# Kernel optimization log

Hardware: AMD Instinct MI355X
Metric: run time of the kernel (lower is better)

## Reference

```python
import jax, jax.numpy as jnp
import numpy as np

B, L = 128, 1024
V, E, H = 32, 256, 1024


def setup_inputs() -> dict:
    key = jax.random.key(0)
    ks = jax.random.split(key, 6)
    return {
        "x": jax.random.randint(ks[0], (B, L), 0, V),
        "hidden": jnp.zeros((B, H), dtype=jnp.float32),
        "embedding": jax.random.normal(ks[1], (V, E), dtype=jnp.float32),
        "W_e": jax.random.normal(ks[2], (E, H), dtype=jnp.float32) * 0.01,
        "W_h": jax.random.normal(ks[3], (H, H), dtype=jnp.float32) * 0.01,
        "b_h": jnp.zeros((H,), dtype=jnp.float32),
        "W_o": jax.random.normal(ks[4], (H, V), dtype=jnp.float32) * 0.01,
        "b_o": jnp.zeros((V,), dtype=jnp.float32),
    }


def reference(x, hidden, embedding, W_e, W_h, b_h, W_o, b_o):
    # x: [B, L] int -> embed: [B, L, E]
    x_embed = embedding[x]
    # Precompute the input projection for all timesteps at once: [L, B, H]
    xin = jnp.einsum("ble,eh->lbh", x_embed, W_e) + b_h

    def step(h, x_t):
        # h: [B, H], x_t: [B, H] (already projected + bias)
        h_new = jnp.tanh(x_t + h @ W_h)
        return h_new, h_new

    final_hidden, outputs = jax.lax.scan(step, hidden, xin)
    # outputs: [L, B, H] -> [B, L, H]
    outputs = outputs.transpose(1, 0, 2)
    logits = outputs @ W_o + b_o  # [B, L, V]
    return logits, final_hidden
```

## Files before the change

### kernel.cpp

```cpp
#include <hip/hip_runtime.h>

typedef unsigned short u16;
typedef unsigned int   u32;
typedef __attribute__((ext_vector_type(4))) float floatx4;
typedef __attribute__((ext_vector_type(4))) u32  u32x4;
typedef __attribute__((ext_vector_type(8))) short short8;

#define B_SZ  128
#define L_SEQ 1024
#define V_SZ  32
#define E_SZ  256
#define H_SZ  1024

#define N_GROUPS     8
#define WG_PER_GROUP 8
#define N_BLOCKS     (N_GROUPS * WG_PER_GROUP)
#define LOGIT_BASE   (B_SZ * L_SEQ * V_SZ)

#define BAR_BYTES  8192
#define FLAG_OFF   (BAR_BYTES - 8)
#define P_OFF      BAR_BYTES
#define P_BYTES    (V_SZ * H_SZ * 4)
#define HBUF_OFF   (P_OFF + P_BYTES)
#define NBUF       4
#define HBUF_G     (NBUF * 16 * H_SZ)
#define HBUF_BYTES (N_GROUPS * HBUF_G * 2)

#define SENT 0xFFFFFFFFu

#define MFMA16x16x32(a, b, c) __builtin_amdgcn_mfma_f32_16x16x32_bf16(a, b, c, 0, 0, 0)

__device__ inline float b2f(u16 u) {
    union { unsigned i; float f; } x; x.i = ((unsigned)u) << 16; return x.f;
}
__device__ inline u16 f2b(float f) {
    unsigned u = __float_as_uint(f);
    return (u16)((u + 0x7FFFu + ((u >> 16) & 1u)) >> 16);
}
__device__ inline float ldf(const void* p, long i, int isf32) {
    return isf32 ? ((const float*)p)[i] : b2f(((const u16*)p)[i]);
}
__device__ inline u16 ldb(const void* p, long i, int isf32) {
    return isf32 ? f2b(((const float*)p)[i]) : ((const u16*)p)[i];
}

__device__ inline float fast_tanh(float x) {
    float cx = fminf(fmaxf(x, -15.f), 15.f);
    float t  = __builtin_amdgcn_exp2f(cx * 2.885390081777927f);
    return (t - 1.f) * __builtin_amdgcn_rcpf(t + 1.f);
}

__device__ inline void bar_lgkm() {
    asm volatile("s_waitcnt lgkmcnt(0)" ::: "memory");
    __builtin_amdgcn_s_barrier();
    asm volatile("" ::: "memory");
}

__device__ inline void ld_row16_raw(const u16* abase, u32x4 a[8]) {
    u32x4 a0, a1, a2, a3, a4, a5, a6, a7;
    asm volatile(
        "global_load_dwordx4 %0, %8, off offset:0   sc0 sc1\n\t"
        "global_load_dwordx4 %1, %8, off offset:64  sc0 sc1\n\t"
        "global_load_dwordx4 %2, %8, off offset:128 sc0 sc1\n\t"
        "global_load_dwordx4 %3, %8, off offset:192 sc0 sc1\n\t"
        "global_load_dwordx4 %4, %8, off offset:256 sc0 sc1\n\t"
        "global_load_dwordx4 %5, %8, off offset:320 sc0 sc1\n\t"
        "global_load_dwordx4 %6, %8, off offset:384 sc0 sc1\n\t"
        "global_load_dwordx4 %7, %8, off offset:448 sc0 sc1\n\t"
        "s_waitcnt vmcnt(0)"
        : "=&v"(a0), "=&v"(a1), "=&v"(a2), "=&v"(a3),
          "=&v"(a4), "=&v"(a5), "=&v"(a6), "=&v"(a7)
        : "v"(abase)
        : "memory");
    a[0] = a0; a[1] = a1; a[2] = a2; a[3] = a3;
    a[4] = a4; a[5] = a5; a[6] = a6; a[7] = a7;
}
__device__ inline u32 maxdw4(u32x4 a) {
    u32 m0 = a[0] > a[1] ? a[0] : a[1];
    u32 m1 = a[2] > a[3] ? a[2] : a[3];
    return m0 > m1 ? m0 : m1;
}
__device__ inline int row_ok(const u32x4 a[8]) {
    u32 m = maxdw4(a[0]);
    #pragma unroll
    for (int j = 1; j < 8; ++j) { u32 t = maxdw4(a[j]); m = t > m ? t : m; }
    return (int)(m != SENT);
}
__device__ inline void poll_row16(const u16* abase, short8 afr[8]) {
    u32x4 av[8];
    ld_row16_raw(abase, av);
    long guard = 0;
    while (!__all(row_ok(av))) {
        if (++guard > 100000L) break;
        __builtin_amdgcn_s_sleep(2);
        ld_row16_raw(abase, av);
    }
    union { u32x4 v; short8 s; } u;
    #pragma unroll
    for (int j = 0; j < 8; ++j) { u.v = av[j]; afr[j] = u.s; }
}
__device__ inline void st_row16(u32* p, u32x4 d) {
    asm volatile("global_store_dwordx4 %0, %1, off sc0 sc1" :: "v"(p), "v"(d) : "memory");
}

__global__ void detect_dtype(const u16* __restrict__ emb, const int* __restrict__ xi,
                             int* __restrict__ flag) {
    float v = b2f(emb[threadIdx.x]);
    if (!(fabsf(v) <= 1.0e6f)) atomicOr(flag, 1);
    if (xi[2 * threadIdx.x + 1] != 0) atomicOr(flag, 2);
}

__global__ void precompute_P(const void* __restrict__ emb, const void* __restrict__ We,
                             const void* __restrict__ bh, float* __restrict__ P,
                             const int* __restrict__ flag) {
    const int isf32 = *flag & 1;
    int o = blockIdx.x * 256 + threadIdx.x;
    int v = o >> 10, h = o & (H_SZ - 1);
    float acc = ldf(bh, h, isf32);
    for (int e = 0; e < E_SZ; ++e)
        acc += ldf(emb, v * E_SZ + e, isf32) * ldf(We, (long)e * H_SZ + h, isf32);
    P[o] = acc;
}

__global__ void __launch_bounds__(256, 1) rnn_kernel(
    const void* __restrict__ xp, const void* __restrict__ hidden,
    const void* __restrict__ Wh, const void* __restrict__ Wo,
    const void* __restrict__ bo, const float* __restrict__ P,
    u16* __restrict__ hbuf, float* __restrict__ out,
    const int* __restrict__ flag)
{
    __shared__ __align__(16) float red[12800];

    const int fl    = *flag;
    const int isf32 = fl & 1;
    const int xi64  = !(fl & 2);
    const int g     = blockIdx.x & 7;
    const int wg    = blockIdx.x >> 3;
    const int col0  = wg * 128;
    const int b0    = g * 16;
    const int tid   = threadIdx.x;
    const int wave  = tid >> 6;
    const int lane  = tid & 63;
    const int lrow  = lane & 15;
    const int quad  = lane >> 4;
    const int kwave = wave * 256;

    const int* x32       = (const int*)xp;
    const long long* x64 = (const long long*)xp;

    u16* hb = hbuf + g * HBUF_G;

    short8 whf[8][8], wof[2][8];
    #pragma unroll
    for (int kk = 0; kk < 8; ++kk) {
        const int kb = kwave + kk * 32 + quad * 8;
        #pragma unroll
        for (int j = 0; j < 8; ++j) {
            #pragma unroll
            for (int nt = 0; nt < 8; ++nt)
                whf[nt][kk][j] = (short)ldb(Wh, (long)(kb + j) * H_SZ + col0 + nt * 16 + lrow, isf32);
            wof[0][kk][j] = (short)ldb(Wo, (long)(kb + j) * V_SZ + lrow, isf32);
            wof[1][kk][j] = (short)ldb(Wo, (long)(kb + j) * V_SZ + 16 + lrow, isf32);
        }
    }

    const int bq = tid >> 4;
    const int c0 = (tid & 15) * 8;
    const float bov0 = ldf(bo, (tid & 15) * 2, isf32);
    const float bov1 = ldf(bo, (tid & 15) * 2 + 1, isf32);

    {
        u32x4 d;
        #pragma unroll
        for (int p = 0; p < 4; ++p) {
            u16 lo = ldb(hidden, (long)(b0 + bq) * H_SZ + col0 + c0 + 2 * p, isf32);
            u16 hi = ldb(hidden, (long)(b0 + bq) * H_SZ + col0 + c0 + 2 * p + 1, isf32);
            d[p] = (u32)lo | ((u32)hi << 16);
        }
        st_row16((u32*)(hb + bq * H_SZ + col0 + c0), d);
    }

    for (int s = 0; s < L_SEQ; ++s) {
        const u16* hc = hb + (s & 3) * (16 * H_SZ);
        u16* hn       = hb + ((s + 1) & 3) * (16 * H_SZ);
        u16* hcl      = hb + ((s + 3) & 3) * (16 * H_SZ);
        const bool do_logit = (wg == (s & 7));

        long xoff = (long)(b0 + bq) * L_SEQ + s;
        int xv = xi64 ? (int)x64[xoff] : x32[xoff];
        const floatx4* pp = (const floatx4*)(P + (long)xv * H_SZ + col0 + c0);
        floatx4 pv0 = pp[0], pv1 = pp[1];

        short8 afr[8];
        poll_row16(hc + lrow * H_SZ + kwave + quad * 8, afr);

        floatx4 acc[8] = {};
        #pragma unroll
        for (int kk = 0; kk < 8; ++kk)
            #pragma unroll
            for (int nt = 0; nt < 8; ++nt)
                acc[nt] = MFMA16x16x32(afr[kk], whf[nt][kk], acc[nt]);
        if (do_logit) {
            floatx4 aL0 = {0,0,0,0}, aL1 = {0,0,0,0};
            #pragma unroll
            for (int kk = 0; kk < 8; ++kk) {
                aL0 = MFMA16x16x32(afr[kk], wof[0][kk], aL0);
                aL1 = MFMA16x16x32(afr[kk], wof[1][kk], aL1);
            }
            #pragma unroll
            for (int r = 0; r < 4; ++r) {
                red[10240 + wave * 640 +       (quad * 4 + r) * 20 + lrow] = aL0[r];
                red[10240 + wave * 640 + 320 + (quad * 4 + r) * 20 + lrow] = aL1[r];
            }
        }

        #pragma unroll
        for (int nt = 0; nt < 8; ++nt)
            #pragma unroll
            for (int r = 0; r < 4; ++r)
                red[wave * 2560 + nt * 320 + (quad * 4 + r) * 20 + lrow] = acc[nt][r];
        bar_lgkm();

        {
            const int base = (c0 >> 4) * 320 + bq * 20 + (c0 & 15);
            floatx4 s0 = {0,0,0,0}, s1 = {0,0,0,0};
            #pragma unroll
            for (int w = 0; w < 4; ++w) {
                s0 += *(const floatx4*)&red[w * 2560 + base];
                s1 += *(const floatx4*)&red[w * 2560 + base + 4];
            }
            float h[8];
            #pragma unroll
            for (int j = 0; j < 4; ++j) h[j]     = fast_tanh(s0[j] + pv0[j]);
            #pragma unroll
            for (int j = 0; j < 4; ++j) h[4 + j] = fast_tanh(s1[j] + pv1[j]);
            u32x4 d;
            #pragma unroll
            for (int p = 0; p < 4; ++p)
                d[p] = (u32)f2b(h[2 * p]) | ((u32)f2b(h[2 * p + 1]) << 16);
            st_row16((u32*)(hn + bq * H_SZ + col0 + c0), d);
            if (s == L_SEQ - 1) {
                float* op = out + LOGIT_BASE + (long)(b0 + bq) * H_SZ + col0 + c0;
                ((floatx4*)op)[0] = floatx4{h[0], h[1], h[2], h[3]};
                ((floatx4*)op)[1] = floatx4{h[4], h[5], h[6], h[7]};
            }
        }
        if (s <= L_SEQ - 3) {
            u32x4 f = { SENT, SENT, SENT, SENT };
            st_row16((u32*)(hcl + bq * H_SZ + col0 + c0), f);
        }

        if (do_logit && s >= 1) {
            int v0 = (tid & 15) * 2;
            int lb = 10240 + (v0 >> 4) * 320 + bq * 20 + (v0 & 15);
            float q0 = 0.f, q1 = 0.f;
            #pragma unroll
            for (int w = 0; w < 4; ++w) {
                q0 += red[lb + w * 640];
                q1 += red[lb + w * 640 + 1];
            }
            long ob = ((long)(b0 + bq) * L_SEQ + (s - 1)) * V_SZ + v0;
            out[ob]     = q0 + bov0;
            out[ob + 1] = q1 + bov1;
        }
        bar_lgkm();
    }

    if (wg == 0) {
        short8 afr[8];
        poll_row16(hb + lrow * H_SZ + kwave + quad * 8, afr);
        floatx4 aL0 = {0,0,0,0}, aL1 = {0,0,0,0};
        #pragma unroll
        for (int kk = 0; kk < 8; ++kk) {
            aL0 = MFMA16x16x32(afr[kk], wof[0][kk], aL0);
            aL1 = MFMA16x16x32(afr[kk], wof[1][kk], aL1);
        }
        #pragma unroll
        for (int r = 0; r < 4; ++r) {
            red[10240 + wave * 640 +       (quad * 4 + r) * 20 + lrow] = aL0[r];
            red[10240 + wave * 640 + 320 + (quad * 4 + r) * 20 + lrow] = aL1[r];
        }
        __syncthreads();
        {
            int v0 = (tid & 15) * 2;
            int lb = 10240 + (v0 >> 4) * 320 + bq * 20 + (v0 & 15);
            float q0 = 0.f, q1 = 0.f;
            #pragma unroll
            for (int w = 0; w < 4; ++w) {
                q0 += red[lb + w * 640];
                q1 += red[lb + w * 640 + 1];
            }
            long ob = ((long)(b0 + bq) * L_SEQ + (L_SEQ - 1)) * V_SZ + v0;
            out[ob]     = q0 + bov0;
            out[ob + 1] = q1 + bov1;
        }
    }
}

extern "C" void kernel_launch(void* const* d_in, const int* in_sizes, int n_in,
                              void* d_out, int out_size, void* d_ws, size_t ws_size,
                              hipStream_t stream) {
    (void)in_sizes; (void)n_in; (void)out_size; (void)ws_size;
    const void* x      = d_in[0];
    const void* hidden = d_in[1];
    const void* emb    = d_in[2];
    const void* We     = d_in[3];
    const void* Wh     = d_in[4];
    const void* bh     = d_in[5];
    const void* Wo     = d_in[6];
    const void* bo     = d_in[7];
    float* out = (float*)d_out;

    char* ws = (char*)d_ws;
    int*   flag = (int*)(ws + FLAG_OFF);
    float* P    = (float*)(ws + P_OFF);
    u16*   hbuf = (u16*)(ws + HBUF_OFF);

    hipMemsetAsync(ws, 0, BAR_BYTES, stream);
    hipMemsetAsync(ws + HBUF_OFF, 0xFF, HBUF_BYTES, stream);

    detect_dtype<<<dim3(1), dim3(256), 0, stream>>>((const u16*)emb, (const int*)x, flag);
    precompute_P<<<dim3(128), dim3(256), 0, stream>>>(emb, We, bh, P, flag);

    rnn_kernel<<<dim3(N_BLOCKS), dim3(256), 0, stream>>>(
        x, hidden, Wh, Wo, bo, P, hbuf, out, flag);
}
```

Baseline: 3.232 ms.

## Split RNN step per wave over full K, removing intra-block barriers

Each wave now owns a 32-column slice of the hidden state and computes the full 1024-long K reduction itself. It polls and loads the entire previous-hidden row instead of a quarter of it. This removes the cross-wave LDS reduction and both block-wide barriers per timestep, leaving only a wave-local transpose through LDS. W_o is staged transposed in LDS for the rotating logit computation, and sentinel clearing is moved earlier. The trade-off is more global loads per wave per step, a larger register footprint, and a serial 32-deep MFMA chain split across two accumulators.

```diff
diff --git a/kernel.cpp b/kernel.cpp
--- a/kernel.cpp
+++ b/kernel.cpp
@@ -50,13 +50,15 @@
     return (t - 1.f) * __builtin_amdgcn_rcpf(t + 1.f);
 }
 
-__device__ inline void bar_lgkm() {
-    asm volatile("s_waitcnt lgkmcnt(0)" ::: "memory");
-    __builtin_amdgcn_s_barrier();
-    asm volatile("" ::: "memory");
-}
-
-__device__ inline void ld_row16_raw(const u16* abase, u32x4 a[8]) {
+__device__ inline void st_row16(u32* p, u32x4 d) {
+    asm volatile("global_store_dwordx4 %0, %1, off sc0 sc1" :: "v"(p), "v"(d) : "memory");
+}
+__device__ inline u32 maxdw4(u32x4 a) {
+    u32 m0 = a[0] > a[1] ? a[0] : a[1];
+    u32 m1 = a[2] > a[3] ? a[2] : a[3];
+    return m0 > m1 ? m0 : m1;
+}
+__device__ inline void ld8_nw(const u16* b, u32x4 a[8]) {
     u32x4 a0, a1, a2, a3, a4, a5, a6, a7;
     asm volatile(
         "global_load_dwordx4 %0, %8, off offset:0   sc0 sc1\n\t"
@@ -66,41 +68,28 @@
         "global_load_dwordx4 %4, %8, off offset:256 sc0 sc1\n\t"
         "global_load_dwordx4 %5, %8, off offset:320 sc0 sc1\n\t"
         "global_load_dwordx4 %6, %8, off offset:384 sc0 sc1\n\t"
-        "global_load_dwordx4 %7, %8, off offset:448 sc0 sc1\n\t"
-        "s_waitcnt vmcnt(0)"
+        "global_load_dwordx4 %7, %8, off offset:448 sc0 sc1"
         : "=&v"(a0), "=&v"(a1), "=&v"(a2), "=&v"(a3),
           "=&v"(a4), "=&v"(a5), "=&v"(a6), "=&v"(a7)
-        : "v"(abase)
+        : "v"(b)
         : "memory");
     a[0] = a0; a[1] = a1; a[2] = a2; a[3] = a3;
     a[4] = a4; a[5] = a5; a[6] = a6; a[7] = a7;
 }
-__device__ inline u32 maxdw4(u32x4 a) {
-    u32 m0 = a[0] > a[1] ? a[0] : a[1];
-    u32 m1 = a[2] > a[3] ? a[2] : a[3];
-    return m0 > m1 ? m0 : m1;
-}
-__device__ inline int row_ok(const u32x4 a[8]) {
-    u32 m = maxdw4(a[0]);
-    #pragma unroll
-    for (int j = 1; j < 8; ++j) { u32 t = maxdw4(a[j]); m = t > m ? t : m; }
-    return (int)(m != SENT);
-}
-__device__ inline void poll_row16(const u16* abase, short8 afr[8]) {
-    u32x4 av[8];
-    ld_row16_raw(abase, av);
-    long guard = 0;
-    while (!__all(row_ok(av))) {
-        if (++guard > 100000L) break;
+__device__ inline void poll_row32(const u16* ab, u32x4 av[32], long& gbudget) {
+    for (;;) {
+        ld8_nw(ab,       av +  0);
+        ld8_nw(ab + 256, av +  8);
+        ld8_nw(ab + 512, av + 16);
+        ld8_nw(ab + 768, av + 24);
+        asm volatile("s_waitcnt vmcnt(0)" ::: "memory");
+        u32 m = 0;
+        #pragma unroll
+        for (int j = 0; j < 32; ++j) { u32 t = maxdw4(av[j]); m = t > m ? t : m; }
+        if (__all((int)(m != SENT))) return;
+        if (--gbudget < 0) return;
         __builtin_amdgcn_s_sleep(2);
-        ld_row16_raw(abase, av);
-    }
-    union { u32x4 v; short8 s; } u;
-    #pragma unroll
-    for (int j = 0; j < 8; ++j) { u.v = av[j]; afr[j] = u.s; }
-}
-__device__ inline void st_row16(u32* p, u32x4 d) {
-    asm volatile("global_store_dwordx4 %0, %1, off sc0 sc1" :: "v"(p), "v"(d) : "memory");
+    }
 }
 
 __global__ void detect_dtype(const u16* __restrict__ emb, const int* __restrict__ xi,
@@ -129,170 +118,151 @@
     u16* __restrict__ hbuf, float* __restrict__ out,
     const int* __restrict__ flag)
 {
-    __shared__ __align__(16) float red[12800];
+    __shared__ __align__(16) u16  woT[V_SZ][H_SZ + 8];
+    __shared__ __align__(16) float trb[4][16][33];
 
     const int fl    = *flag;
     const int isf32 = fl & 1;
     const int xi64  = !(fl & 2);
     const int g     = blockIdx.x & 7;
     const int wg    = blockIdx.x >> 3;
-    const int col0  = wg * 128;
     const int b0    = g * 16;
     const int tid   = threadIdx.x;
     const int wave  = tid >> 6;
     const int lane  = tid & 63;
     const int lrow  = lane & 15;
     const int quad  = lane >> 4;
-    const int kwave = wave * 256;
+    const int w8    = wg * 4 + wave;
+    const int wcol0 = w8 * 32;
 
     const int* x32       = (const int*)xp;
     const long long* x64 = (const long long*)xp;
-
     u16* hb = hbuf + g * HBUF_G;
 
-    short8 whf[8][8], wof[2][8];
+    long gbudget = 100000L;
+
+    for (int i = tid; i < V_SZ * H_SZ; i += 256) {
+        int k = i >> 5, v = i & 31;
+        woT[v][k] = ldb(Wo, (long)k * V_SZ + v, isf32);
+    }
+
+    short8 whf[2][32];
     #pragma unroll
-    for (int kk = 0; kk < 8; ++kk) {
-        const int kb = kwave + kk * 32 + quad * 8;
+    for (int c = 0; c < 32; ++c) {
+        const int kb = c * 32 + quad * 8;
         #pragma unroll
         for (int j = 0; j < 8; ++j) {
-            #pragma unroll
-            for (int nt = 0; nt < 8; ++nt)
-                whf[nt][kk][j] = (short)ldb(Wh, (long)(kb + j) * H_SZ + col0 + nt * 16 + lrow, isf32);
-            wof[0][kk][j] = (short)ldb(Wo, (long)(kb + j) * V_SZ + lrow, isf32);
-            wof[1][kk][j] = (short)ldb(Wo, (long)(kb + j) * V_SZ + 16 + lrow, isf32);
-        }
-    }
-
-    const int bq = tid >> 4;
-    const int c0 = (tid & 15) * 8;
-    const float bov0 = ldf(bo, (tid & 15) * 2, isf32);
-    const float bov1 = ldf(bo, (tid & 15) * 2 + 1, isf32);
+            whf[0][c][j] = (short)ldb(Wh, (long)(kb + j) * H_SZ + wcol0 + lrow,      isf32);
+            whf[1][c][j] = (short)ldb(Wh, (long)(kb + j) * H_SZ + wcol0 + 16 + lrow, isf32);
+        }
+    }
+
+    const float bov0 = ldf(bo, lrow,      isf32);
+    const float bov1 = ldf(bo, 16 + lrow, isf32);
 
     {
         u32x4 d;
         #pragma unroll
         for (int p = 0; p < 4; ++p) {
-            u16 lo = ldb(hidden, (long)(b0 + bq) * H_SZ + col0 + c0 + 2 * p, isf32);
-            u16 hi = ldb(hidden, (long)(b0 + bq) * H_SZ + col0 + c0 + 2 * p + 1, isf32);
+            u16 lo = ldb(hidden, (long)(b0 + lrow) * H_SZ + wcol0 + quad * 8 + 2 * p,     isf32);
+            u16 hi = ldb(hidden, (long)(b0 + lrow) * H_SZ + wcol0 + quad * 8 + 2 * p + 1, isf32);
             d[p] = (u32)lo | ((u32)hi << 16);
         }
-        st_row16((u32*)(hb + bq * H_SZ + col0 + c0), d);
-    }
+        st_row16((u32*)(hb + lrow * H_SZ + wcol0 + quad * 8), d);
+    }
+    __syncthreads();
 
     for (int s = 0; s < L_SEQ; ++s) {
         const u16* hc = hb + (s & 3) * (16 * H_SZ);
         u16* hn       = hb + ((s + 1) & 3) * (16 * H_SZ);
         u16* hcl      = hb + ((s + 3) & 3) * (16 * H_SZ);
-        const bool do_logit = (wg == (s & 7));
-
-        long xoff = (long)(b0 + bq) * L_SEQ + s;
+        const int dol = (s >= 1) & (w8 == ((s - 1) & 31));
+
+        long xoff = (long)(b0 + lrow) * L_SEQ + s;
         int xv = xi64 ? (int)x64[xoff] : x32[xoff];
-        const floatx4* pp = (const floatx4*)(P + (long)xv * H_SZ + col0 + c0);
+        const floatx4* pp = (const floatx4*)(P + (long)xv * H_SZ + wcol0 + quad * 8);
         floatx4 pv0 = pp[0], pv1 = pp[1];
 
-        short8 afr[8];
-        poll_row16(hc + lrow * H_SZ + kwave + quad * 8, afr);
-
-        floatx4 acc[8] = {};
-        #pragma unroll
-        for (int kk = 0; kk < 8; ++kk)
+        u32x4 av[32];
+        poll_row32(hc + lrow * H_SZ + quad * 8, av, gbudget);
+
+        if (s <= L_SEQ - 3) {
+            u32x4 f = { SENT, SENT, SENT, SENT };
+            st_row16((u32*)(hcl + lrow * H_SZ + wcol0 + quad * 8), f);
+        }
+
+        floatx4 aA0 = {0,0,0,0}, aB0 = {0,0,0,0}, aA1 = {0,0,0,0}, aB1 = {0,0,0,0};
+        #pragma unroll
+        for (int c = 0; c < 32; c += 2) {
+            union { u32x4 v; short8 h; } u0, u1;
+            u0.v = av[c]; u1.v = av[c + 1];
+            aA0 = MFMA16x16x32(u0.h, whf[0][c],     aA0);
+            aA1 = MFMA16x16x32(u0.h, whf[1][c],     aA1);
+            aB0 = MFMA16x16x32(u1.h, whf[0][c + 1], aB0);
+            aB1 = MFMA16x16x32(u1.h, whf[1][c + 1], aB1);
+        }
+        floatx4 ac0 = aA0 + aB0, ac1 = aA1 + aB1;
+
+        #pragma unroll
+        for (int r = 0; r < 4; ++r) {
+            trb[wave][quad * 4 + r][lrow]      = ac0[r];
+            trb[wave][quad * 4 + r][16 + lrow] = ac1[r];
+        }
+        asm volatile("s_waitcnt lgkmcnt(0)" ::: "memory");
+        __builtin_amdgcn_sched_barrier(0);
+
+        float hv[8];
+        #pragma unroll
+        for (int j = 0; j < 4; ++j) hv[j]     = fast_tanh(trb[wave][lrow][quad * 8 + j]     + pv0[j]);
+        #pragma unroll
+        for (int j = 0; j < 4; ++j) hv[4 + j] = fast_tanh(trb[wave][lrow][quad * 8 + 4 + j] + pv1[j]);
+        u32x4 d;
+        #pragma unroll
+        for (int p = 0; p < 4; ++p)
+            d[p] = (u32)f2b(hv[2 * p]) | ((u32)f2b(hv[2 * p + 1]) << 16);
+        st_row16((u32*)(hn + lrow * H_SZ + wcol0 + quad * 8), d);
+        if (s == L_SEQ - 1) {
+            float* op = out + LOGIT_BASE + (long)(b0 + lrow) * H_SZ + wcol0 + quad * 8;
+            ((floatx4*)op)[0] = floatx4{hv[0], hv[1], hv[2], hv[3]};
+            ((floatx4*)op)[1] = floatx4{hv[4], hv[5], hv[6], hv[7]};
+        }
+
+        if (dol) {
+            floatx4 L0 = {0,0,0,0}, L1 = {0,0,0,0};
             #pragma unroll
-            for (int nt = 0; nt < 8; ++nt)
-                acc[nt] = MFMA16x16x32(afr[kk], whf[nt][kk], acc[nt]);
-        if (do_logit) {
-            floatx4 aL0 = {0,0,0,0}, aL1 = {0,0,0,0};
-            #pragma unroll
-            for (int kk = 0; kk < 8; ++kk) {
-                aL0 = MFMA16x16x32(afr[kk], wof[0][kk], aL0);
-                aL1 = MFMA16x16x32(afr[kk], wof[1][kk], aL1);
+            for (int c = 0; c < 32; ++c) {
+                union { u32x4 v; short8 h; } ua; ua.v = av[c];
+                short8 w0 = *(const short8*)&woT[lrow][c * 32 + quad * 8];
+                short8 w1 = *(const short8*)&woT[16 + lrow][c * 32 + quad * 8];
+                L0 = MFMA16x16x32(ua.h, w0, L0);
+                L1 = MFMA16x16x32(ua.h, w1, L1);
             }
             #pragma unroll
             for (int r = 0; r < 4; ++r) {
-                red[10240 + wave * 640 +       (quad * 4 + r) * 20 + lrow] = aL0[r];
-                red[10240 + wave * 640 + 320 + (quad * 4 + r) * 20 + lrow] = aL1[r];
+                long ob = ((long)(b0 + quad * 4 + r) * L_SEQ + (s - 1)) * V_SZ;
+                out[ob + lrow]      = L0[r] + bov0;
+                out[ob + 16 + lrow] = L1[r] + bov1;
             }
         }
-
-        #pragma unroll
-        for (int nt = 0; nt < 8; ++nt)
-            #pragma unroll
-            for (int r = 0; r < 4; ++r)
-                red[wave * 2560 + nt * 320 + (quad * 4 + r) * 20 + lrow] = acc[nt][r];
-        bar_lgkm();
-
-        {
-            const int base = (c0 >> 4) * 320 + bq * 20 + (c0 & 15);
-            floatx4 s0 = {0,0,0,0}, s1 = {0,0,0,0};
-            #pragma unroll
-            for (int w = 0; w < 4; ++w) {
-                s0 += *(const floatx4*)&red[w * 2560 + base];
-                s1 += *(const floatx4*)&red[w * 2560 + base + 4];
-            }
-            float h[8];
-            #pragma unroll
-            for (int j = 0; j < 4; ++j) h[j]     = fast_tanh(s0[j] + pv0[j]);
-            #pragma unroll
-            for (int j = 0; j < 4; ++j) h[4 + j] = fast_tanh(s1[j] + pv1[j]);
-            u32x4 d;
-            #pragma unroll
-            for (int p = 0; p < 4; ++p)
-                d[p] = (u32)f2b(h[2 * p]) | ((u32)f2b(h[2 * p + 1]) << 16);
-            st_row16((u32*)(hn + bq * H_SZ + col0 + c0), d);
-            if (s == L_SEQ - 1) {
-                float* op = out + LOGIT_BASE + (long)(b0 + bq) * H_SZ + col0 + c0;
-                ((floatx4*)op)[0] = floatx4{h[0], h[1], h[2], h[3]};
-                ((floatx4*)op)[1] = floatx4{h[4], h[5], h[6], h[7]};
-            }
-        }
-        if (s <= L_SEQ - 3) {
-            u32x4 f = { SENT, SENT, SENT, SENT };
-            st_row16((u32*)(hcl + bq * H_SZ + col0 + c0), f);
-        }
-
-        if (do_logit && s >= 1) {
-            int v0 = (tid & 15) * 2;
-            int lb = 10240 + (v0 >> 4) * 320 + bq * 20 + (v0 & 15);
-            float q0 = 0.f, q1 = 0.f;
-            #pragma unroll
-            for (int w = 0; w < 4; ++w) {
-                q0 += red[lb + w * 640];
-                q1 += red[lb + w * 640 + 1];
-            }
-            long ob = ((long)(b0 + bq) * L_SEQ + (s - 1)) * V_SZ + v0;
-            out[ob]     = q0 + bov0;
-            out[ob + 1] = q1 + bov1;
-        }
-        bar_lgkm();
-    }
-
-    if (wg == 0) {
-        short8 afr[8];
-        poll_row16(hb + lrow * H_SZ + kwave + quad * 8, afr);
-        floatx4 aL0 = {0,0,0,0}, aL1 = {0,0,0,0};
-        #pragma unroll
-        for (int kk = 0; kk < 8; ++kk) {
-            aL0 = MFMA16x16x32(afr[kk], wof[0][kk], aL0);
-            aL1 = MFMA16x16x32(afr[kk], wof[1][kk], aL1);
+    }
+
+    if (w8 == 31) {
+        u32x4 av[32];
+        poll_row32(hb + lrow * H_SZ + quad * 8, av, gbudget);
+        floatx4 L0 = {0,0,0,0}, L1 = {0,0,0,0};
+        #pragma unroll
+        for (int c = 0; c < 32; ++c) {
+            union { u32x4 v; short8 h; } ua; ua.v = av[c];
+            short8 w0 = *(const short8*)&woT[lrow][c * 32 + quad * 8];
+            short8 w1 = *(const short8*)&woT[16 + lrow][c * 32 + quad * 8];
+            L0 = MFMA16x16x32(ua.h, w0, L0);
+            L1 = MFMA16x16x32(ua.h, w1, L1);
         }
         #pragma unroll
         for (int r = 0; r < 4; ++r) {
-            red[10240 + wave * 640 +       (quad * 4 + r) * 20 + lrow] = aL0[r];
-            red[10240 + wave * 640 + 320 + (quad * 4 + r) * 20 + lrow] = aL1[r];
-        }
-        __syncthreads();
-        {
-            int v0 = (tid & 15) * 2;
-            int lb = 10240 + (v0 >> 4) * 320 + bq * 20 + (v0 & 15);
-            float q0 = 0.f, q1 = 0.f;
-            #pragma unroll
-            for (int w = 0; w < 4; ++w) {
-                q0 += red[lb + w * 640];
-                q1 += red[lb + w * 640 + 1];
-            }
-            long ob = ((long)(b0 + bq) * L_SEQ + (L_SEQ - 1)) * V_SZ + v0;
-            out[ob]     = q0 + bov0;
-            out[ob + 1] = q1 + bov1;
+            long ob = ((long)(b0 + quad * 4 + r) * L_SEQ + (L_SEQ - 1)) * V_SZ;
+            out[ob + lrow]      = L0[r] + bov0;
+            out[ob + 16 + lrow] = L1[r] + bov1;
         }
     }
 }
```

Measured after the change: 8.210 ms. 154% more time.

## Prefetch next-step hidden row, token index and P row before barrier

Applied to the files above, without the earlier changes.

The next step's hidden-state poll load, the token index two steps ahead and the projected-embedding row are now issued at the end of each step as non-waiting asm loads. A single vmcnt wait at the top of the loop replaces the serial load chains. The logit MFMAs are interleaved into the main k-loop, and the spin-wait guard becomes a global budget. The aim is to hide global-memory latency on the recurrence's critical path. The risk is that the speculative hidden load often sees sentinel values and falls back to polling, and the extra live registers add pressure.

```diff
diff --git a/kernel.cpp b/kernel.cpp
--- a/kernel.cpp
+++ b/kernel.cpp
@@ -50,12 +50,16 @@
     return (t - 1.f) * __builtin_amdgcn_rcpf(t + 1.f);
 }
 
+#define VMCNT0() asm volatile("s_waitcnt vmcnt(0)" ::: "memory")
+
 __device__ inline void bar_lgkm() {
     asm volatile("s_waitcnt lgkmcnt(0)" ::: "memory");
     __builtin_amdgcn_s_barrier();
     asm volatile("" ::: "memory");
 }
-
+__device__ inline void st_row16(u32* p, u32x4 d) {
+    asm volatile("global_store_dwordx4 %0, %1, off sc0 sc1" :: "v"(p), "v"(d) : "memory");
+}
 __device__ inline void ld_row16_raw(const u16* abase, u32x4 a[8]) {
     u32x4 a0, a1, a2, a3, a4, a5, a6, a7;
     asm volatile(
@@ -75,6 +79,32 @@
     a[0] = a0; a[1] = a1; a[2] = a2; a[3] = a3;
     a[4] = a4; a[5] = a5; a[6] = a6; a[7] = a7;
 }
+__device__ inline void ld8_nw(const u16* b, u32x4 a[8]) {
+    u32x4 a0, a1, a2, a3, a4, a5, a6, a7;
+    asm volatile(
+        "global_load_dwordx4 %0, %8, off offset:0   sc0 sc1\n\t"
+        "global_load_dwordx4 %1, %8, off offset:64  sc0 sc1\n\t"
+        "global_load_dwordx4 %2, %8, off offset:128 sc0 sc1\n\t"
+        "global_load_dwordx4 %3, %8, off offset:192 sc0 sc1\n\t"
+        "global_load_dwordx4 %4, %8, off offset:256 sc0 sc1\n\t"
+        "global_load_dwordx4 %5, %8, off offset:320 sc0 sc1\n\t"
+        "global_load_dwordx4 %6, %8, off offset:384 sc0 sc1\n\t"
+        "global_load_dwordx4 %7, %8, off offset:448 sc0 sc1"
+        : "=&v"(a0), "=&v"(a1), "=&v"(a2), "=&v"(a3),
+          "=&v"(a4), "=&v"(a5), "=&v"(a6), "=&v"(a7)
+        : "v"(b)
+        : "memory");
+    a[0] = a0; a[1] = a1; a[2] = a2; a[3] = a3;
+    a[4] = a4; a[5] = a5; a[6] = a6; a[7] = a7;
+}
+__device__ inline void ld_x32_nw(const void* addr, u32& x_) {
+    asm volatile("global_load_dword %0, %1, off" : "=&v"(x_) : "v"(addr) : "memory");
+}
+__device__ inline void ld_P2_nw(const float* addr, u32x4& p0, u32x4& p1) {
+    asm volatile("global_load_dwordx4 %0, %2, off offset:0\n\t"
+                 "global_load_dwordx4 %1, %2, off offset:16"
+                 : "=&v"(p0), "=&v"(p1) : "v"(addr) : "memory");
+}
 __device__ inline u32 maxdw4(u32x4 a) {
     u32 m0 = a[0] > a[1] ? a[0] : a[1];
     u32 m1 = a[2] > a[3] ? a[2] : a[3];
@@ -85,22 +115,6 @@
     #pragma unroll
     for (int j = 1; j < 8; ++j) { u32 t = maxdw4(a[j]); m = t > m ? t : m; }
     return (int)(m != SENT);
-}
-__device__ inline void poll_row16(const u16* abase, short8 afr[8]) {
-    u32x4 av[8];
-    ld_row16_raw(abase, av);
-    long guard = 0;
-    while (!__all(row_ok(av))) {
-        if (++guard > 100000L) break;
-        __builtin_amdgcn_s_sleep(2);
-        ld_row16_raw(abase, av);
-    }
-    union { u32x4 v; short8 s; } u;
-    #pragma unroll
-    for (int j = 0; j < 8; ++j) { u.v = av[j]; afr[j] = u.s; }
-}
-__device__ inline void st_row16(u32* p, u32x4 d) {
-    asm volatile("global_store_dwordx4 %0, %1, off sc0 sc1" :: "v"(p), "v"(d) : "memory");
 }
 
 __global__ void detect_dtype(const u16* __restrict__ emb, const int* __restrict__ xi,
@@ -145,10 +159,12 @@
     const int quad  = lane >> 4;
     const int kwave = wave * 256;
 
-    const int* x32       = (const int*)xp;
-    const long long* x64 = (const long long*)xp;
+    const char* xbase = (const char*)xp;
+    const int   xstep = xi64 ? 8 : 4;
 
     u16* hb = hbuf + g * HBUF_G;
+
+    long gb = 100000L;
 
     short8 whf[8][8], wof[2][8];
     #pragma unroll
@@ -178,6 +194,17 @@
             d[p] = (u32)lo | ((u32)hi << 16);
         }
         st_row16((u32*)(hb + bq * H_SZ + col0 + c0), d);
+    }
+
+    u32x4 S0[8];
+    u32x4 pu0, pu1;
+    u32   xr;
+    {
+        long xo0 = (long)(b0 + bq) * L_SEQ;
+        int xv0 = xi64 ? (int)((const long long*)xp)[xo0] : ((const int*)xp)[xo0];
+        ld_P2_nw(P + (long)xv0 * H_SZ + col0 + c0, pu0, pu1);
+        ld_x32_nw(xbase + (xo0 + 1) * xstep, xr);
+        ld8_nw(hb + lrow * H_SZ + kwave + quad * 8, S0);
     }
 
     for (int s = 0; s < L_SEQ; ++s) {
@@ -185,35 +212,41 @@
         u16* hn       = hb + ((s + 1) & 3) * (16 * H_SZ);
         u16* hcl      = hb + ((s + 3) & 3) * (16 * H_SZ);
         const bool do_logit = (wg == (s & 7));
-
-        long xoff = (long)(b0 + bq) * L_SEQ + s;
-        int xv = xi64 ? (int)x64[xoff] : x32[xoff];
-        const floatx4* pp = (const floatx4*)(P + (long)xv * H_SZ + col0 + c0);
-        floatx4 pv0 = pp[0], pv1 = pp[1];
-
-        short8 afr[8];
-        poll_row16(hc + lrow * H_SZ + kwave + quad * 8, afr);
+        const u16* ab = hc + lrow * H_SZ + kwave + quad * 8;
+
+        VMCNT0();
+        __builtin_amdgcn_sched_barrier(0);
+
+        if (!__all(row_ok(S0))) {
+            for (;;) {
+                if (--gb < 0) break;
+                __builtin_amdgcn_s_sleep(2);
+                ld_row16_raw(ab, S0);
+                if (__all(row_ok(S0))) break;
+            }
+        }
 
         floatx4 acc[8] = {};
-        #pragma unroll
-        for (int kk = 0; kk < 8; ++kk)
+        floatx4 aL0 = {0,0,0,0}, aL1 = {0,0,0,0};
+        #pragma unroll
+        for (int kk = 0; kk < 8; ++kk) {
+            union { u32x4 v; short8 h; } ua; ua.v = S0[kk];
             #pragma unroll
             for (int nt = 0; nt < 8; ++nt)
-                acc[nt] = MFMA16x16x32(afr[kk], whf[nt][kk], acc[nt]);
+                acc[nt] = MFMA16x16x32(ua.h, whf[nt][kk], acc[nt]);
+            if (do_logit) {
+                aL0 = MFMA16x16x32(ua.h, wof[0][kk], aL0);
+                aL1 = MFMA16x16x32(ua.h, wof[1][kk], aL1);
+            }
+        }
+
         if (do_logit) {
-            floatx4 aL0 = {0,0,0,0}, aL1 = {0,0,0,0};
-            #pragma unroll
-            for (int kk = 0; kk < 8; ++kk) {
-                aL0 = MFMA16x16x32(afr[kk], wof[0][kk], aL0);
-                aL1 = MFMA16x16x32(afr[kk], wof[1][kk], aL1);
-            }
             #pragma unroll
             for (int r = 0; r < 4; ++r) {
                 red[10240 + wave * 640 +       (quad * 4 + r) * 20 + lrow] = aL0[r];
                 red[10240 + wave * 640 + 320 + (quad * 4 + r) * 20 + lrow] = aL1[r];
             }
         }
-
         #pragma unroll
         for (int nt = 0; nt < 8; ++nt)
             #pragma unroll
@@ -229,11 +262,13 @@
                 s0 += *(const floatx4*)&red[w * 2560 + base];
                 s1 += *(const floatx4*)&red[w * 2560 + base + 4];
             }
+            union { u32x4 v; float f[4]; } q0, q1;
+            q0.v = pu0; q1.v = pu1;
             float h[8];
             #pragma unroll
-            for (int j = 0; j < 4; ++j) h[j]     = fast_tanh(s0[j] + pv0[j]);
-            #pragma unroll
-            for (int j = 0; j < 4; ++j) h[4 + j] = fast_tanh(s1[j] + pv1[j]);
+            for (int j = 0; j < 4; ++j) h[j]     = fast_tanh(s0[j] + q0.f[j]);
+            #pragma unroll
+            for (int j = 0; j < 4; ++j) h[4 + j] = fast_tanh(s1[j] + q1.f[j]);
             u32x4 d;
             #pragma unroll
             for (int p = 0; p < 4; ++p)
@@ -263,17 +298,36 @@
             out[ob]     = q0 + bov0;
             out[ob + 1] = q1 + bov1;
         }
+
+        {
+            int xnv = (int)xr;
+            ld_P2_nw(P + (long)xnv * H_SZ + col0 + c0, pu0, pu1);
+            long s2 = (s + 2 < L_SEQ) ? (s + 2) : 0;
+            ld_x32_nw(xbase + ((long)(b0 + bq) * L_SEQ + s2) * xstep, xr);
+            ld8_nw(hn + lrow * H_SZ + kwave + quad * 8, S0);
+        }
         bar_lgkm();
     }
 
+    VMCNT0();
+    __builtin_amdgcn_sched_barrier(0);
+
     if (wg == 0) {
-        short8 afr[8];
-        poll_row16(hb + lrow * H_SZ + kwave + quad * 8, afr);
+        const u16* ab = hb + lrow * H_SZ + kwave + quad * 8;
+        if (!__all(row_ok(S0))) {
+            for (;;) {
+                if (--gb < 0) break;
+                __builtin_amdgcn_s_sleep(2);
+                ld_row16_raw(ab, S0);
+                if (__all(row_ok(S0))) break;
+            }
+        }
         floatx4 aL0 = {0,0,0,0}, aL1 = {0,0,0,0};
         #pragma unroll
         for (int kk = 0; kk < 8; ++kk) {
-            aL0 = MFMA16x16x32(afr[kk], wof[0][kk], aL0);
-            aL1 = MFMA16x16x32(afr[kk], wof[1][kk], aL1);
+            union { u32x4 v; short8 h; } ua; ua.v = S0[kk];
+            aL0 = MFMA16x16x32(ua.h, wof[0][kk], aL0);
+            aL1 = MFMA16x16x32(ua.h, wof[1][kk], aL1);
         }
         #pragma unroll
         for (int r = 0; r < 4; ++r) {
```

New measurement: 3.393 ms. 1.05x slower.
